# Kernel optimization log

Measured on AMD Instinct MI355X. Metric: run time of the kernel, lower is better.

## Reference

```python
import jax, jax.numpy as jnp
import numpy as np

N, E = 50000, 800000
F_IN, HID, HEADS = 128, 32, 8
H1 = HID * HEADS            # 256: conv1 concat output, also conv2 in/out
NUM_WALKS, WALK_LEN = 512, 64
WINDOW, NEG_S = 5, 10
TEMP = 0.07
NEG_SLOPE = 0.2


def setup_inputs() -> dict:
    key = jax.random.key(0)
    ks = jax.random.split(key, 16)
    inp = {
        "x": jax.random.normal(ks[0], (N, F_IN), jnp.float32),
        "edge_index": jax.random.randint(ks[1], (2, E), 0, N),
        "walks": jax.random.randint(ks[2], (NUM_WALKS, WALK_LEN), 0, N),
        "neg_nodes": jax.random.randint(ks[3], (NUM_WALKS, WALK_LEN, NEG_S), 0, N),
        # conv1 params (GATConv: in=F_IN, out=HID, heads=HEADS, concat)
        "W1": jax.random.normal(ks[4], (F_IN, HEADS * HID), jnp.float32) / np.sqrt(F_IN),
        "a_src1": jax.random.normal(ks[5], (HEADS, HID), jnp.float32) / np.sqrt(HID),
        "a_dst1": jax.random.normal(ks[6], (HEADS, HID), jnp.float32) / np.sqrt(HID),
        "b1": jnp.zeros((HEADS * HID,), jnp.float32),
        # conv2 params (GATConv: in=H1, out=H1, heads=1)
        "W2": jax.random.normal(ks[7], (H1, H1), jnp.float32) / np.sqrt(H1),
        "a_src2": jax.random.normal(ks[8], (1, H1), jnp.float32) / np.sqrt(H1),
        "a_dst2": jax.random.normal(ks[9], (1, H1), jnp.float32) / np.sqrt(H1),
        "b2": jnp.zeros((H1,), jnp.float32),
    }
    return inp


def gat_conv(x, edge_index, W, a_src, a_dst, b, heads, out_ch):
    """PyG-style GATConv: self-loops, per-dst softmax attention, concat heads."""
    n = x.shape[0]
    loops = jnp.arange(n)
    src = jnp.concatenate([edge_index[0], loops])
    dst = jnp.concatenate([edge_index[1], loops])
    xw = (x @ W).reshape(n, heads, out_ch)                  # [N,H,C]
    al_s = jnp.einsum('nhc,hc->nh', xw, a_src)              # [N,H]
    al_d = jnp.einsum('nhc,hc->nh', xw, a_dst)
    e = jax.nn.leaky_relu(al_s[src] + al_d[dst], NEG_SLOPE)  # [Et,H]
    m = jax.ops.segment_max(e, dst, num_segments=n)
    ex = jnp.exp(e - m[dst])
    den = jax.ops.segment_sum(ex, dst, num_segments=n)
    alpha = ex / den[dst]                                    # [Et,H]
    out = jax.ops.segment_sum(alpha[:, :, None] * xw[src], dst, num_segments=n)
    return out.reshape(n, heads * out_ch) + b


def walk_contrastive_loss(emb, walks, neg_nodes):
    eps = 1e-8
    nrm = emb / jnp.clip(jnp.linalg.norm(emb, axis=-1, keepdims=True), eps)
    L = walks.shape[1]
    offs = jnp.concatenate([jnp.arange(-WINDOW, 0), jnp.arange(1, WINDOW + 1)])  # [2W]
    pos_pos = jnp.arange(L)[:, None] + offs[None, :]        # [L,2W]
    pos_valid = (pos_pos >= 0) & (pos_pos < L)
    pos_nodes = walks[:, jnp.clip(pos_pos, 0, L - 1)]       # [B,L,2W]
    anchor = nrm[walks]                                      # [B,L,D]
    pos_sims = jnp.einsum('bld,blpd->blp', anchor, nrm[pos_nodes]) / TEMP
    neg_sims = jnp.einsum('bld,blsd->bls', anchor, nrm[neg_nodes]) / TEMP
    # drop negatives that collide with (valid) positives, as torch.isin filter does
    neg_in_pos = ((neg_nodes[:, :, :, None] == pos_nodes[:, :, None, :])
                  & pos_valid[None, :, None, :]).any(-1)     # [B,L,S]
    pos_sum = jnp.sum(jnp.exp(pos_sims) * pos_valid[None].astype(emb.dtype), axis=-1)
    neg_sum = jnp.sum(jnp.exp(neg_sims) * (~neg_in_pos).astype(emb.dtype), axis=-1)
    has_pos = pos_valid.any(-1)[None]                        # [1,L]
    safe_pos = jnp.where(has_pos, pos_sum, 1.0)
    term = -jnp.log(safe_pos / (safe_pos + neg_sum))
    return jnp.sum(jnp.where(has_pos, term, 0.0))


def reference(x, edge_index, walks, neg_nodes, W1, a_src1, a_dst1, b1,
              W2, a_src2, a_dst2, b2):
    emb1 = jax.nn.elu(gat_conv(x, edge_index, W1, a_src1, a_dst1, b1, HEADS, HID))
    emb2 = gat_conv(emb1, edge_index, W2, a_src2, a_dst2, b2, 1, H1)
    emb = jnp.concatenate([emb1, emb2], axis=1)              # [N, 2*H1]
    return walk_contrastive_loss(emb, walks, neg_nodes)
```

## Files before the change

kernel.cpp:

```cpp
#include <hip/hip_runtime.h>
#include <math.h>

#define N_NODES 50000
#define N_PAD 50048
#define E_EDGES 800000
#define E_PAD (E_EDGES + 8 * N_NODES)
#define FDIM_IN 128
#define HID_1 32
#define HEADS_1 8
#define H1DIM 256
#define NUM_WALKS 512
#define WALK_LEN 64
#define WINDOW 5
#define NEG_S 10
#define TEMP 0.07f
#define INV_TEMP (1.0f / 0.07f)
#define NEG_SLOPE 0.2f
#define LOG2E 1.44269504f

#define SCAN_BLOCKS ((N_NODES + 255) / 256)

typedef unsigned int uint;
typedef unsigned short ushort;
typedef long long i64_t;
typedef __attribute__((ext_vector_type(8))) short bf16x8;
typedef __attribute__((ext_vector_type(8))) ushort us8;
typedef __attribute__((ext_vector_type(4))) float f32x4;
typedef __attribute__((ext_vector_type(2))) float vf2;
typedef __attribute__((ext_vector_type(2))) i64_t i64x2;

__device__ __forceinline__ float leaky(float v) {
    return fmaxf(v, v * NEG_SLOPE);
}

__device__ __forceinline__ float bfl(uint u) { return __uint_as_float(u << 16); }
__device__ __forceinline__ float bfh(uint u) { return __uint_as_float(u & 0xffff0000u); }

__device__ __forceinline__ ushort f2bf(float x) {
    uint u = __float_as_uint(x);
    u = u + 0x7fffu + ((u >> 16) & 1u);
    return (ushort)(u >> 16);
}

__device__ __forceinline__ uint pk4fp8(float a, float b, float c, float d) {
    int u = __builtin_amdgcn_cvt_pk_fp8_f32(a, b, 0, false);
    u = __builtin_amdgcn_cvt_pk_fp8_f32(c, d, u, true);
    return (uint)u;
}

__device__ __forceinline__ float red16(float x) {
    int v = __float_as_int(x);
    x += __int_as_float(__builtin_amdgcn_update_dpp(0, v, 0xB1, 0xF, 0xF, true));
    v = __float_as_int(x);
    x += __int_as_float(__builtin_amdgcn_update_dpp(0, v, 0x4E, 0xF, 0xF, true));
    v = __float_as_int(x);
    x += __int_as_float(__builtin_amdgcn_update_dpp(0, v, 0x141, 0xF, 0xF, true));
    v = __float_as_int(x);
    x += __int_as_float(__builtin_amdgcn_update_dpp(0, v, 0x140, 0xF, 0xF, true));
    return x;
}


#define PB_CVT  6250
#define PB_DEG  3125
#define PB_FILL ((E_PAD / 2 + 255) / 256)
#define PO_DEG  (PB_CVT)
#define PO_FILL (PO_DEG + PB_DEG)
#define PO_WT1  (PO_FILL + PB_FILL)
#define PO_WT2  (PO_WT1 + 128)
#define PO_MISC (PO_WT2 + 256)
#define PREP_GRID (PO_MISC + 1)

__global__ __launch_bounds__(256) void prep_kernel(
        const float* __restrict__ x, const int* __restrict__ ei,
        const float* __restrict__ W1, const float* __restrict__ W2,
        uint* __restrict__ xb, ushort* __restrict__ wt1, ushort* __restrict__ wt2,
        int* __restrict__ deg, uint* __restrict__ srl_u,
        float* __restrict__ als1, float* __restrict__ als2, uint* __restrict__ xw8) {
    const int blk = blockIdx.x, t = threadIdx.x;
    if (blk < PB_CVT) {
        int i = blk * 256 + t;
        float4 v = ((const float4*)x)[i];
        uint2 p;
        p.x = (uint)f2bf(v.x) | ((uint)f2bf(v.y) << 16);
        p.y = (uint)f2bf(v.z) | ((uint)f2bf(v.w) << 16);
        ((uint2*)xb)[i] = p;
    } else if (blk < PO_FILL) {
        int e = (blk - PO_DEG) * 256 + t;
        atomicAdd(&deg[ei[E_EDGES + e]], 1);
    } else if (blk < PO_WT1) {
        int i = (blk - PO_FILL) * 256 + t;
        if (i < E_PAD / 2) srl_u[i] = 0xC350C350u;
    } else if (blk < PO_WT2) {
        int tid = (blk - PO_WT1) * 256 + t;
        int k = tid >> 8, n = tid & 255;
        wt1[n * 128 + k] = f2bf(W1[k * 256 + n]);
    } else if (blk < PO_MISC) {
        int tid = (blk - PO_WT2) * 256 + t;
        int k = tid >> 8, n = tid & 255;
        wt2[n * 256 + k] = f2bf(W2[k * 256 + n]);
    } else {
        if (t < HEADS_1) als1[N_NODES * HEADS_1 + t] = -1e30f;
        if (t == HEADS_1) als2[N_NODES] = -1e30f;
        if (t >= 64 && t < 128) xw8[N_NODES * 64 + (t - 64)] = 0u;
    }
}


__global__ __launch_bounds__(256) void scan_a(const int* __restrict__ deg,
                                              int* __restrict__ excl,
                                              int* __restrict__ bsum) {
    __shared__ int s[256];
    int t = threadIdx.x;
    int i = blockIdx.x * 256 + t;
    int d = (i < N_NODES) ? deg[i] : 0;
    int v = (d + 7) & ~7;
    s[t] = v;
    __syncthreads();
    for (int off = 1; off < 256; off <<= 1) {
        int tmp = (t >= off) ? s[t - off] : 0;
        __syncthreads();
        s[t] += tmp;
        __syncthreads();
    }
    if (i < N_NODES) excl[i] = s[t] - v;
    if (t == 255) bsum[blockIdx.x] = s[255];
}

__global__ __launch_bounds__(256) void scan_b(int* __restrict__ bsum) {
    __shared__ int s[256];
    int t = threadIdx.x;
    int v = (t < SCAN_BLOCKS) ? bsum[t] : 0;
    s[t] = v;
    __syncthreads();
    for (int off = 1; off < 256; off <<= 1) {
        int tmp = (t >= off) ? s[t - off] : 0;
        __syncthreads();
        s[t] += tmp;
        __syncthreads();
    }
    if (t < SCAN_BLOCKS) bsum[t] = s[t] - v;
}

__global__ void scan_c2(const int* __restrict__ deg,
                        int* __restrict__ excl, const int* __restrict__ bsum,
                        int* __restrict__ row_start) {
    int i = blockIdx.x * blockDim.x + threadIdx.x;
    if (i < N_NODES) {
        int rs = excl[i] + bsum[i >> 8];
        row_start[i] = rs;
        if (i == N_NODES - 1) row_start[N_NODES] = rs + ((deg[i] + 7) & ~7);
    }
}

__global__ void bucket_kernel(const int* __restrict__ ei,
                              const int* __restrict__ row_start,
                              int* __restrict__ cursor,
                              ushort* __restrict__ srclist) {
    int e = blockIdx.x * blockDim.x + threadIdx.x;
    if (e >= E_EDGES) return;
    int dst = ei[E_EDGES + e];
    int pos = atomicAdd(&cursor[dst], 1);
    srclist[row_start[dst] + pos] = (ushort)ei[e];
}

template<int K, int H>
__global__ __launch_bounds__(256) void mfma_gemm64(
        const ushort* __restrict__ A,
        const ushort* __restrict__ Wt,
        uint* __restrict__ Y8,
        const float* __restrict__ a_src,
        const float* __restrict__ a_dst,
        float* __restrict__ als, float* __restrict__ ald) {
    constexpr int KP = K + 8;
    constexpr int K8 = K / 8;
    __shared__ __align__(16) ushort As[64 * KP];
    __shared__ float sals[64][5], sald[64][5];
    const int m0 = blockIdx.x * 64;
    const int t = threadIdx.x;
    const uint4* Ag = (const uint4*)(A + (size_t)m0 * K);
    uint4* As4 = (uint4*)As;
    for (int i = t; i < 64 * K8; i += 256) {
        int r = i / K8, c8 = i % K8;
        As4[r * (K8 + 1) + c8] = Ag[i];
    }
    __syncthreads();
    const int wv = __builtin_amdgcn_readfirstlane(t >> 6);
    const int lane = t & 63;
    const int n0 = wv * 64;
    const int mrow = lane & 15, q = lane >> 4;
    f32x4 acc[4][4];
#pragma unroll
    for (int mt = 0; mt < 4; mt++)
#pragma unroll
        for (int i = 0; i < 4; i++) acc[mt][i] = (f32x4){0.f, 0.f, 0.f, 0.f};
#pragma unroll
    for (int k0 = 0; k0 < K; k0 += 32) {
        bf16x8 a[4], b[4];
#pragma unroll
        for (int mt = 0; mt < 4; mt++)
            a[mt] = *(const bf16x8*)(As + (mt * 16 + mrow) * KP + k0 + q * 8);
#pragma unroll
        for (int i = 0; i < 4; i++)
            b[i] = *(const bf16x8*)(Wt + (uint)(n0 + i * 16 + mrow) * K + k0 + q * 8);
#pragma unroll
        for (int mt = 0; mt < 4; mt++)
#pragma unroll
            for (int i = 0; i < 4; i++)
                acc[mt][i] = __builtin_amdgcn_mfma_f32_16x16x32_bf16(a[mt], b[i], acc[mt][i], 0, 0, 0);
    }
    {
        float as[4], ad[4];
#pragma unroll
        for (int i = 0; i < 4; i++) {
            as[i] = a_src[n0 + i * 16 + mrow];
            ad[i] = a_dst[n0 + i * 16 + mrow];
        }
#pragma unroll
        for (int mt = 0; mt < 4; mt++) {
#pragma unroll
            for (int r = 0; r < 4; r++) {
                const int row = m0 + mt * 16 + q * 4 + r;
                if (H == 8) {
                    float ps0 = acc[mt][0][r] * as[0] + acc[mt][1][r] * as[1];
                    float ps1 = acc[mt][2][r] * as[2] + acc[mt][3][r] * as[3];
                    float pd0 = acc[mt][0][r] * ad[0] + acc[mt][1][r] * ad[1];
                    float pd1 = acc[mt][2][r] * ad[2] + acc[mt][3][r] * ad[3];
#pragma unroll
                    for (int o = 1; o < 16; o <<= 1) {
                        ps0 += __shfl_xor(ps0, o, 64); ps1 += __shfl_xor(ps1, o, 64);
                        pd0 += __shfl_xor(pd0, o, 64); pd1 += __shfl_xor(pd1, o, 64);
                    }
                    if (mrow == 0 && row < N_NODES) {
                        als[row * 8 + 2 * wv] = ps0 * LOG2E;
                        als[row * 8 + 2 * wv + 1] = ps1 * LOG2E;
                        ald[row * 8 + 2 * wv] = pd0 * LOG2E;
                        ald[row * 8 + 2 * wv + 1] = pd1 * LOG2E;
                    }
                } else {
                    float ps = acc[mt][0][r] * as[0] + acc[mt][1][r] * as[1]
                             + acc[mt][2][r] * as[2] + acc[mt][3][r] * as[3];
                    float pd = acc[mt][0][r] * ad[0] + acc[mt][1][r] * ad[1]
                             + acc[mt][2][r] * ad[2] + acc[mt][3][r] * ad[3];
#pragma unroll
                    for (int o = 1; o < 16; o <<= 1) {
                        ps += __shfl_xor(ps, o, 64); pd += __shfl_xor(pd, o, 64);
                    }
                    if (mrow == 0) {
                        sals[mt * 16 + q * 4 + r][wv] = ps;
                        sald[mt * 16 + q * 4 + r][wv] = pd;
                    }
                }
            }
        }
    }
    __syncthreads();
    if (H == 1 && t < 64) {
        const int row = m0 + t;
        if (row < N_NODES) {
            als[row] = (sals[t][0] + sals[t][1] + sals[t][2] + sals[t][3]) * LOG2E;
            ald[row] = (sald[t][0] + sald[t][1] + sald[t][2] + sald[t][3]) * LOG2E;
        }
    }
    float* S = (float*)As + wv * 16 * 68;
    const int prow = lane >> 2, pj = lane & 3;
#pragma unroll
    for (int mt = 0; mt < 4; mt++) {
#pragma unroll
        for (int i = 0; i < 4; i++)
#pragma unroll
            for (int r = 0; r < 4; r++)
                S[(q * 4 + r) * 68 + i * 16 + mrow] = acc[mt][i][r];
        const float* cp = S + prow * 68 + pj * 16;
        uint4 o;
        o.x = pk4fp8(cp[0],  cp[1],  cp[2],  cp[3]);
        o.y = pk4fp8(cp[4],  cp[5],  cp[6],  cp[7]);
        o.z = pk4fp8(cp[8],  cp[9],  cp[10], cp[11]);
        o.w = pk4fp8(cp[12], cp[13], cp[14], cp[15]);
        const int row = m0 + mt * 16 + prow;
        if (row < N_NODES)
            ((uint4*)(Y8 + (size_t)row * 64))[wv * 4 + pj] = o;
    }
}

__global__ __launch_bounds__(256) void gat_gather1(
        const int* __restrict__ row_start, const ushort* __restrict__ srclist,
        const float* __restrict__ als, const float* __restrict__ ald,
        const uint* __restrict__ xw8,
        const float* __restrict__ bias,
        ushort* __restrict__ emb1b) {
    const int wid = __builtin_amdgcn_readfirstlane(blockIdx.x * 4 + (threadIdx.x >> 6));
    const uint lane = threadIdx.x & 63;
    const uint h = lane >> 3;
    const float ald_n = ald[wid * HEADS_1 + h];
    const int beg = row_start[wid], end = row_start[wid + 1];

    float ex0 = __builtin_amdgcn_exp2f(leaky(als[wid * HEADS_1 + h] + ald_n));
    uint u = xw8[((uint)wid << 6) + lane];
    vf2 lo = __builtin_amdgcn_cvt_pk_f32_fp8((int)u, false);
    vf2 hi = __builtin_amdgcn_cvt_pk_f32_fp8((int)u, true);
    float den = ex0;
    vf2 exv0 = {ex0, ex0};
    vf2 a01 = exv0 * lo, a23 = exv0 * hi;

    for (int i = beg; i < end; i += 8) {
        us8 sv = *(const us8*)(srclist + i);
        uint rr[8]; float ee[8];
#pragma unroll
        for (int j = 0; j < 8; j++) rr[j] = xw8[((uint)sv[j] << 6) + lane];
#pragma unroll
        for (int j = 0; j < 8; j++) ee[j] = als[(uint)sv[j] * HEADS_1 + h];
#pragma unroll
        for (int j = 0; j < 8; j++) {
            float ex = __builtin_amdgcn_exp2f(leaky(ee[j] + ald_n));
            vf2 l2 = __builtin_amdgcn_cvt_pk_f32_fp8((int)rr[j], false);
            vf2 h2 = __builtin_amdgcn_cvt_pk_f32_fp8((int)rr[j], true);
            den += ex;
            vf2 exv = {ex, ex};
            a01 += exv * l2;
            a23 += exv * h2;
        }
    }
    float inv = 1.f / den;
    float4 bv = ((const float4*)bias)[lane];
    float4 r;
    r.x = a01[0] * inv + bv.x; r.y = a01[1] * inv + bv.y;
    r.z = a23[0] * inv + bv.z; r.w = a23[1] * inv + bv.w;
    r.x = r.x > 0.f ? r.x : __expf(r.x) - 1.f;
    r.y = r.y > 0.f ? r.y : __expf(r.y) - 1.f;
    r.z = r.z > 0.f ? r.z : __expf(r.z) - 1.f;
    r.w = r.w > 0.f ? r.w : __expf(r.w) - 1.f;
    uint2 p;
    p.x = (uint)f2bf(r.x) | ((uint)f2bf(r.y) << 16);
    p.y = (uint)f2bf(r.z) | ((uint)f2bf(r.w) << 16);
    ((uint2*)emb1b)[((uint)wid << 6) + lane] = p;
}

__global__ __launch_bounds__(256) void gat_gather2(
        const int* __restrict__ row_start, const ushort* __restrict__ srclist,
        const float* __restrict__ als, const float* __restrict__ ald,
        const uint* __restrict__ xw8,
        const float* __restrict__ bias,
        const ushort* __restrict__ emb1b,
        uint* __restrict__ embn8) {
    const int wid = __builtin_amdgcn_readfirstlane(blockIdx.x * 4 + (threadIdx.x >> 6));
    const uint lane = threadIdx.x & 63;
    const float ald_n = ald[wid];
    const int beg = row_start[wid], end = row_start[wid + 1];

    float ex0 = __builtin_amdgcn_exp2f(leaky(als[wid] + ald_n));
    uint u = xw8[((uint)wid << 6) + lane];
    vf2 lo = __builtin_amdgcn_cvt_pk_f32_fp8((int)u, false);
    vf2 hi = __builtin_amdgcn_cvt_pk_f32_fp8((int)u, true);
    float den = ex0;
    vf2 exv0 = {ex0, ex0};
    vf2 a01 = exv0 * lo, a23 = exv0 * hi;

    for (int i = beg; i < end; i += 8) {
        us8 sv = *(const us8*)(srclist + i);
        uint rr[8]; float ee[8];
#pragma unroll
        for (int j = 0; j < 8; j++) rr[j] = xw8[((uint)sv[j] << 6) + lane];
#pragma unroll
        for (int j = 0; j < 8; j++) ee[j] = als[(uint)sv[j]];
#pragma unroll
        for (int j = 0; j < 8; j++) {
            float ex = __builtin_amdgcn_exp2f(leaky(ee[j] + ald_n));
            vf2 l2 = __builtin_amdgcn_cvt_pk_f32_fp8((int)rr[j], false);
            vf2 h2 = __builtin_amdgcn_cvt_pk_f32_fp8((int)rr[j], true);
            den += ex;
            vf2 exv = {ex, ex};
            a01 += exv * l2;
            a23 += exv * h2;
        }
    }
    float inv = 1.f / den;
    float4 bv = ((const float4*)bias)[lane];
    float4 e2;
    e2.x = a01[0] * inv + bv.x; e2.y = a01[1] * inv + bv.y;
    e2.z = a23[0] * inv + bv.z; e2.w = a23[1] * inv + bv.w;
    uint2 u1 = ((const uint2*)emb1b)[((uint)wid << 6) + lane];
    float4 e1;
    e1.x = bfl(u1.x); e1.y = bfh(u1.x); e1.z = bfl(u1.y); e1.w = bfh(u1.y);

    float ssum = e1.x * e1.x + e1.y * e1.y + e1.z * e1.z + e1.w * e1.w
               + e2.x * e2.x + e2.y * e2.y + e2.z * e2.z + e2.w * e2.w;
#pragma unroll
    for (int o = 32; o > 0; o >>= 1) ssum += __shfl_xor(ssum, o, 64);
    float innv = 1.f / fmaxf(sqrtf(ssum), 1e-8f);

    uint p1 = pk4fp8(e1.x * innv, e1.y * innv, e1.z * innv, e1.w * innv);
    uint p2 = pk4fp8(e2.x * innv, e2.y * innv, e2.z * innv, e2.w * innv);
    const uint n1 = ((lane >> 4) << 4) | (((lane >> 1) & 3) << 2) | (((lane >> 3) & 1) << 1) | (lane & 1);
    embn8[((uint)wid << 7) + n1] = p1;
    embn8[((uint)wid << 7) + 64 + n1] = p2;
}


#define ROWU 140

__global__ __launch_bounds__(1024, 8) void loss_mfma_kernel(
        const uint* __restrict__ embn8,
        const int* __restrict__ walks, const int* __restrict__ negs,
        float* __restrict__ out) {
    __shared__ __align__(16) uint srows8[WALK_LEN * ROWU];
    __shared__ int wids[WALK_LEN];
    __shared__ float possum[WALK_LEN];
    __shared__ float negsum[WALK_LEN];
    const int b = blockIdx.x;
    const int t = threadIdx.x;
    const int w = __builtin_amdgcn_readfirstlane(t >> 6);
    const int lane = t & 63;
    const int mrow = lane & 15, q = lane >> 4;
    const char* embc = (const char*)embn8;

    if (t < 64) wids[t] = walks[b * WALK_LEN + t];
    else if (t < 128) possum[t - 64] = 0.f;
    else if (t < 192) negsum[t - 128] = 0.f;

    uint4 Bv[8];
    int pnode = negs[b * (WALK_LEN * NEG_S) + (w * 16 + mrow)];
    {
        const char* bp = embc + (((uint)pnode) << 9) + (uint)(q * 16);
#pragma unroll
        for (int j = 0; j < 8; j++) Bv[j] = *(const uint4*)(bp + j * 64);
    }
    __syncthreads();

    {
        const int rA = w * 4 + (lane >> 5);
        const int rB = rA + 2;
        const uint off = lane & 31;
        ((uint4*)(srows8 + rA * ROWU))[off] = ((const uint4*)embn8)[((uint)wids[rA] << 5) + off];
        ((uint4*)(srows8 + rB * ROWU))[off] = ((const uint4*)embn8)[((uint)wids[rB] << 5) + off];
    }
    __syncthreads();

#pragma unroll
    for (int ji = 0; ji < 3; ji++) {
        const int job = w + ji * 16;
        f32x4 acc0 = {0.f, 0.f, 0.f, 0.f};
        f32x4 acc1 = {0.f, 0.f, 0.f, 0.f};
        if (ji < 2 || w < 8) {
            const int albase = (job / 10) * 16;
            const int curnode = pnode;
            const int owner = (job * 16 + mrow) / 10;
            const char* ap = (const char*)(srows8 + (albase + mrow) * ROWU) + q * 16;
#pragma unroll
            for (int j = 0; j < 4; j++) {
                i64x2 a = *(const i64x2*)(ap + j * 64);
                const i64x2 bb = *(const i64x2*)&Bv[j];
                acc0 = __builtin_amdgcn_mfma_f32_16x16x32_fp8_fp8(a[0], bb[0], acc0, 0, 0, 0);
                acc0 = __builtin_amdgcn_mfma_f32_16x16x32_fp8_fp8(a[1], bb[1], acc0, 0, 0, 0);
            }
#pragma unroll
            for (int j = 4; j < 8; j++) {
                i64x2 a = *(const i64x2*)(ap + j * 64);
                const i64x2 bb = *(const i64x2*)&Bv[j];
                acc1 = __builtin_amdgcn_mfma_f32_16x16x32_fp8_fp8(a[0], bb[0], acc1, 0, 0, 0);
                acc1 = __builtin_amdgcn_mfma_f32_16x16x32_fp8_fp8(a[1], bb[1], acc1, 0, 0, 0);
            }
            if (ji == 0 || (ji == 1 && w < 8)) {
                const int njob = job + 16;
                pnode = negs[b * (WALK_LEN * NEG_S) + (njob * 16 + mrow)];
                const char* bp = embc + (((uint)pnode) << 9) + (uint)(q * 16);
#pragma unroll
                for (int j = 0; j < 8; j++) Bv[j] = *(const uint4*)(bp + j * 64);
            }
#pragma unroll
            for (int reg = 0; reg < 4; reg++) {
                const int l_a = albase + q * 4 + reg;
                float e = 0.f;
                if (owner == l_a) {
                    bool msk = false;
#pragma unroll
                    for (int dj = -WINDOW; dj <= WINDOW; dj++) {
                        if (dj == 0) continue;
                        int p = l_a + dj;
                        if (p >= 0 && p < WALK_LEN && wids[p] == curnode) msk = true;
                    }
                    if (!msk) e = __expf((acc0[reg] + acc1[reg]) * INV_TEMP);
                }
                e = red16(e);
                if (mrow == 0 && e != 0.f) atomicAdd(&negsum[l_a], e);
            }
        } else {
            const int pj = w - 8;
            const int g = pj >> 1, half = pj & 1;
            const int albase = g * 16;
            const int base = (albase - WINDOW) > 0 ? (albase - WINDOW) : 0;
            const int hi = (albase + 15 + WINDOW) < (WALK_LEN - 1) ? (albase + 15 + WINDOW) : (WALK_LEN - 1);
            const int cnt = hi - base + 1;
            const int r = half * 16 + mrow;
            const int row = base + r;
            const int rc = row < hi ? row : hi;
            const char* ap = (const char*)(srows8 + (albase + mrow) * ROWU) + q * 16;
            const char* bp = (const char*)(srows8 + rc * ROWU) + q * 16;
#pragma unroll
            for (int j = 0; j < 4; j++) {
                i64x2 a = *(const i64x2*)(ap + j * 64);
                i64x2 bb = *(const i64x2*)(bp + j * 64);
                acc0 = __builtin_amdgcn_mfma_f32_16x16x32_fp8_fp8(a[0], bb[0], acc0, 0, 0, 0);
                acc0 = __builtin_amdgcn_mfma_f32_16x16x32_fp8_fp8(a[1], bb[1], acc0, 0, 0, 0);
            }
#pragma unroll
            for (int j = 4; j < 8; j++) {
                i64x2 a = *(const i64x2*)(ap + j * 64);
                i64x2 bb = *(const i64x2*)(bp + j * 64);
                acc1 = __builtin_amdgcn_mfma_f32_16x16x32_fp8_fp8(a[0], bb[0], acc1, 0, 0, 0);
                acc1 = __builtin_amdgcn_mfma_f32_16x16x32_fp8_fp8(a[1], bb[1], acc1, 0, 0, 0);
            }
#pragma unroll
            for (int reg = 0; reg < 4; reg++) {
                const int l_a = albase + q * 4 + reg;
                const int d = row - l_a;
                bool use = (r < cnt) && (d != 0) && (d >= -WINDOW) && (d <= WINDOW);
                float e = use ? __expf((acc0[reg] + acc1[reg]) * INV_TEMP) : 0.f;
                e = red16(e);
                if (mrow == 0 && e != 0.f) atomicAdd(&possum[l_a], e);
            }
        }
    }
    __syncthreads();
    if (t < 64) {
        float term = logf(1.f + negsum[t] / possum[t]);
#pragma unroll
        for (int o = 32; o > 0; o >>= 1) term += __shfl_xor(term, o, 64);
        if (t == 0) atomicAdd(out, term);
    }
}

extern "C" void kernel_launch(void* const* d_in, const int* in_sizes, int n_in,
                              void* d_out, int out_size, void* d_ws, size_t ws_size,
                              hipStream_t stream) {
    const float* x      = (const float*)d_in[0];
    const int*   ei     = (const int*)d_in[1];
    const int*   walks  = (const int*)d_in[2];
    const int*   negs   = (const int*)d_in[3];
    const float* W1     = (const float*)d_in[4];
    const float* a_src1 = (const float*)d_in[5];
    const float* a_dst1 = (const float*)d_in[6];
    const float* b1     = (const float*)d_in[7];
    const float* W2     = (const float*)d_in[8];
    const float* a_src2 = (const float*)d_in[9];
    const float* a_dst2 = (const float*)d_in[10];
    const float* b2     = (const float*)d_in[11];
    float* out = (float*)d_out;

    float* ws = (float*)d_ws;
    size_t off = 0;
#define ALIGN_OFF off = (off + 255) & ~(size_t)255
    float* r_xw8   = ws + off; off += (size_t)(N_NODES + 1) * 64;  ALIGN_OFF;
    float* r_emb1b = ws + off; off += (size_t)N_PAD * 128;         ALIGN_OFF;
    float* r_embn8 = ws + off; off += (size_t)N_NODES * 128;       ALIGN_OFF;
    float* r_xb    = ws + off; off += (size_t)N_PAD * 64;          ALIGN_OFF;
    float* r_wt1   = ws + off; off += 256 * 64;                    ALIGN_OFF;
    float* r_wt2   = ws + off; off += 256 * 128;                   ALIGN_OFF;
    float* als1  = ws + off; off += (N_NODES + 1) * HEADS_1;       ALIGN_OFF;
    float* ald1  = ws + off; off += N_NODES * HEADS_1;             ALIGN_OFF;
    float* als2  = ws + off; off += N_NODES + 1;                   ALIGN_OFF;
    float* ald2  = ws + off; off += N_NODES;                       ALIGN_OFF;
    int* deg       = (int*)(ws + off); off += N_NODES;             ALIGN_OFF;
    int* excl      = (int*)(ws + off); off += N_NODES;             ALIGN_OFF;
    int* bsum      = (int*)(ws + off); off += 256;                 ALIGN_OFF;
    int* row_start = (int*)(ws + off); off += N_NODES + 1;         ALIGN_OFF;
    int* cursor    = (int*)(ws + off); off += N_NODES;             ALIGN_OFF;
    ushort* srclist = (ushort*)(ws + off); off += E_PAD / 2;       ALIGN_OFF;
    uint*   xw8   = (uint*)r_xw8;
    ushort* emb1b = (ushort*)r_emb1b;
    uint*   embn8 = (uint*)r_embn8;
    ushort* xb    = (ushort*)r_xb;
    ushort* wt1   = (ushort*)r_wt1;
    ushort* wt2   = (ushort*)r_wt2;

    hipMemsetAsync(out, 0, sizeof(float) * out_size, stream);
    hipMemsetAsync(deg, 0, sizeof(int) * N_NODES, stream);
    hipMemsetAsync(cursor, 0, sizeof(int) * N_NODES, stream);

    prep_kernel<<<PREP_GRID, 256, 0, stream>>>(
        x, ei, W1, W2, (uint*)xb, wt1, wt2, deg, (uint*)srclist, als1, als2, xw8);

    scan_a<<<SCAN_BLOCKS, 256, 0, stream>>>(deg, excl, bsum);
    scan_b<<<1, 256, 0, stream>>>(bsum);
    scan_c2<<<SCAN_BLOCKS, 256, 0, stream>>>(deg, excl, bsum, row_start);
    bucket_kernel<<<(E_EDGES + 255) / 256, 256, 0, stream>>>(ei, row_start, cursor, srclist);

    mfma_gemm64<128, HEADS_1><<<N_PAD / 64, 256, 0, stream>>>(
        xb, wt1, xw8, a_src1, a_dst1, als1, ald1);
    gat_gather1<<<N_NODES / 4, 256, 0, stream>>>(
        row_start, srclist, als1, ald1, xw8, b1, emb1b);

    mfma_gemm64<256, 1><<<N_PAD / 64, 256, 0, stream>>>(
        emb1b, wt2, xw8, a_src2, a_dst2, als2, ald2);
    gat_gather2<<<N_NODES / 4, 256, 0, stream>>>(
        row_start, srclist, als2, ald2, xw8, b2, emb1b, embn8);

    loss_mfma_kernel<<<NUM_WALKS, 1024, 0, stream>>>(embn8, walks, negs, out);
}
```

Baseline: 346.8 us.

## Fuse edge bucketing into first GEMM launch with dst-range partitioned blocks

```diff
diff --git a/kernel.cpp b/kernel.cpp
--- a/kernel.cpp
+++ b/kernel.cpp
@@ -19,6 +19,12 @@
 #define LOG2E 1.44269504f
 
 #define SCAN_BLOCKS ((N_NODES + 255) / 256)
+
+#define NCHUNK 3125
+#define NSTRIPE 196
+#define NGEMMG 98
+#define NGROUP1 (NSTRIPE + NGEMMG)
+#define GEMM1_GRID (NGROUP1 * 8)
 
 typedef unsigned int uint;
 typedef unsigned short ushort;
@@ -144,24 +150,14 @@
 
 __global__ void scan_c2(const int* __restrict__ deg,
                         int* __restrict__ excl, const int* __restrict__ bsum,
-                        int* __restrict__ row_start) {
+                        int* __restrict__ row_start, int* __restrict__ cursor) {
     int i = blockIdx.x * blockDim.x + threadIdx.x;
     if (i < N_NODES) {
         int rs = excl[i] + bsum[i >> 8];
         row_start[i] = rs;
+        cursor[i] = rs;
         if (i == N_NODES - 1) row_start[N_NODES] = rs + ((deg[i] + 7) & ~7);
     }
-}
-
-__global__ void bucket_kernel(const int* __restrict__ ei,
-                              const int* __restrict__ row_start,
-                              int* __restrict__ cursor,
-                              ushort* __restrict__ srclist) {
-    int e = blockIdx.x * blockDim.x + threadIdx.x;
-    if (e >= E_EDGES) return;
-    int dst = ei[E_EDGES + e];
-    int pos = atomicAdd(&cursor[dst], 1);
-    srclist[row_start[dst] + pos] = (ushort)ei[e];
 }
 
 template<int K, int H>
@@ -171,12 +167,43 @@
         uint* __restrict__ Y8,
         const float* __restrict__ a_src,
         const float* __restrict__ a_dst,
-        float* __restrict__ als, float* __restrict__ ald) {
+        float* __restrict__ als, float* __restrict__ ald,
+        const int* __restrict__ ei, int* __restrict__ cursor,
+        ushort* __restrict__ srclist) {
     constexpr int KP = K + 8;
     constexpr int K8 = K / 8;
     __shared__ __align__(16) ushort As[64 * KP];
     __shared__ float sals[64][5], sald[64][5];
-    const int m0 = blockIdx.x * 64;
+    int m0;
+    if (H == 8) {
+        const int G = blockIdx.x >> 3;
+        if (G % 3 != 0) {
+            const int stripe = G - G / 3 - 1;
+            const int lo = (blockIdx.x & 7) * (N_NODES / 8);
+            int dstv[16], srcv[16];
+#pragma unroll
+            for (int j = 0; j < 16; j++) {
+                int chunk = stripe + j * NSTRIPE;
+                bool ok = chunk < NCHUNK;
+                int e = chunk * 256 + threadIdx.x;
+                dstv[j] = ok ? ei[E_EDGES + e] : -1;
+                srcv[j] = ok ? ei[e] : 0;
+            }
+#pragma unroll
+            for (int j = 0; j < 16; j++) {
+                if ((uint)(dstv[j] - lo) < (uint)(N_NODES / 8)) {
+                    int pos = atomicAdd(&cursor[dstv[j]], 1);
+                    srclist[pos] = (ushort)srcv[j];
+                }
+            }
+            return;
+        }
+        const int job = (G / 3) * 8 + (blockIdx.x & 7);
+        if (job >= N_PAD / 64) return;
+        m0 = job * 64;
+    } else {
+        m0 = blockIdx.x * 64;
+    }
     const int t = threadIdx.x;
     const uint4* Ag = (const uint4*)(A + (size_t)m0 * K);
     uint4* As4 = (uint4*)As;
@@ -575,23 +602,21 @@
 
     hipMemsetAsync(out, 0, sizeof(float) * out_size, stream);
     hipMemsetAsync(deg, 0, sizeof(int) * N_NODES, stream);
-    hipMemsetAsync(cursor, 0, sizeof(int) * N_NODES, stream);
 
     prep_kernel<<<PREP_GRID, 256, 0, stream>>>(
         x, ei, W1, W2, (uint*)xb, wt1, wt2, deg, (uint*)srclist, als1, als2, xw8);
 
     scan_a<<<SCAN_BLOCKS, 256, 0, stream>>>(deg, excl, bsum);
     scan_b<<<1, 256, 0, stream>>>(bsum);
-    scan_c2<<<SCAN_BLOCKS, 256, 0, stream>>>(deg, excl, bsum, row_start);
-    bucket_kernel<<<(E_EDGES + 255) / 256, 256, 0, stream>>>(ei, row_start, cursor, srclist);
-
-    mfma_gemm64<128, HEADS_1><<<N_PAD / 64, 256, 0, stream>>>(
-        xb, wt1, xw8, a_src1, a_dst1, als1, ald1);
+    scan_c2<<<SCAN_BLOCKS, 256, 0, stream>>>(deg, excl, bsum, row_start, cursor);
+
+    mfma_gemm64<128, HEADS_1><<<GEMM1_GRID, 256, 0, stream>>>(
+        xb, wt1, xw8, a_src1, a_dst1, als1, ald1, ei, cursor, srclist);
     gat_gather1<<<N_NODES / 4, 256, 0, stream>>>(
         row_start, srclist, als1, ald1, xw8, b1, emb1b);
 
     mfma_gemm64<256, 1><<<N_PAD / 64, 256, 0, stream>>>(
-        emb1b, wt2, xw8, a_src2, a_dst2, als2, ald2);
+        emb1b, wt2, xw8, a_src2, a_dst2, als2, ald2, ei, cursor, srclist);
     gat_gather2<<<N_NODES / 4, 256, 0, stream>>>(
         row_start, srclist, als2, ald2, xw8, b2, emb1b, embn8);
 
```

Result: faster. 328.6 us (-5.3%).

## Replace atomic CSR bucket fill with two-pass binned scatter via LDS windows

Applied to the files above, without the earlier changes.

```diff
diff --git a/kernel.cpp b/kernel.cpp
--- a/kernel.cpp
+++ b/kernel.cpp
@@ -20,6 +20,12 @@
 
 #define SCAN_BLOCKS ((N_NODES + 255) / 256)
 
+#define NB 98
+#define GCAP 12288
+#define LCAP 64
+#define BIN_BLOCKS 392
+#define WINCAP 16384
+
 typedef unsigned int uint;
 typedef unsigned short ushort;
 typedef long long i64_t;
@@ -28,6 +34,7 @@
 typedef __attribute__((ext_vector_type(4))) float f32x4;
 typedef __attribute__((ext_vector_type(2))) float vf2;
 typedef __attribute__((ext_vector_type(2))) i64_t i64x2;
+typedef __attribute__((ext_vector_type(4))) uint u32x4;
 
 __device__ __forceinline__ float leaky(float v) {
     return fmaxf(v, v * NEG_SLOPE);
@@ -62,20 +69,15 @@
 
 
 #define PB_CVT  6250
-#define PB_DEG  3125
-#define PB_FILL ((E_PAD / 2 + 255) / 256)
-#define PO_DEG  (PB_CVT)
-#define PO_FILL (PO_DEG + PB_DEG)
-#define PO_WT1  (PO_FILL + PB_FILL)
+#define PO_WT1  (PB_CVT)
 #define PO_WT2  (PO_WT1 + 128)
 #define PO_MISC (PO_WT2 + 256)
 #define PREP_GRID (PO_MISC + 1)
 
 __global__ __launch_bounds__(256) void prep_kernel(
-        const float* __restrict__ x, const int* __restrict__ ei,
+        const float* __restrict__ x,
         const float* __restrict__ W1, const float* __restrict__ W2,
         uint* __restrict__ xb, ushort* __restrict__ wt1, ushort* __restrict__ wt2,
-        int* __restrict__ deg, uint* __restrict__ srl_u,
         float* __restrict__ als1, float* __restrict__ als2, uint* __restrict__ xw8) {
     const int blk = blockIdx.x, t = threadIdx.x;
     if (blk < PB_CVT) {
@@ -85,12 +87,6 @@
         p.x = (uint)f2bf(v.x) | ((uint)f2bf(v.y) << 16);
         p.y = (uint)f2bf(v.z) | ((uint)f2bf(v.w) << 16);
         ((uint2*)xb)[i] = p;
-    } else if (blk < PO_FILL) {
-        int e = (blk - PO_DEG) * 256 + t;
-        atomicAdd(&deg[ei[E_EDGES + e]], 1);
-    } else if (blk < PO_WT1) {
-        int i = (blk - PO_FILL) * 256 + t;
-        if (i < E_PAD / 2) srl_u[i] = 0xC350C350u;
     } else if (blk < PO_WT2) {
         int tid = (blk - PO_WT1) * 256 + t;
         int k = tid >> 8, n = tid & 255;
@@ -107,6 +103,49 @@
 }
 
 
+__global__ __launch_bounds__(256) void bin_kernel(
+        const int* __restrict__ ei, int* __restrict__ deg,
+        uint* __restrict__ gbucket, int* __restrict__ gcur) {
+    __shared__ int scnt[NB];
+    __shared__ int gposs[NB];
+    __shared__ uint sbuf[NB * LCAP];
+    const int t = threadIdx.x;
+    if (t < NB) scnt[t] = 0;
+    __syncthreads();
+    const int e0 = blockIdx.x * 2048;
+#pragma unroll
+    for (int k = 0; k < 8; k++) {
+        int e = e0 + k * 256 + t;
+        if (e < E_EDGES) {
+            int dst = ei[E_EDGES + e];
+            int src = ei[e];
+            atomicAdd(&deg[dst], 1);
+            uint packed = ((uint)dst << 16) | (uint)src;
+            int bk = dst >> 9;
+            int pos = atomicAdd(&scnt[bk], 1);
+            if (pos < LCAP) sbuf[bk * LCAP + pos] = packed;
+            else {
+                int gp = atomicAdd(&gcur[bk], 1);
+                gbucket[bk * GCAP + gp] = packed;
+            }
+        }
+    }
+    __syncthreads();
+    if (t < NB) {
+        int c = scnt[t]; if (c > LCAP) c = LCAP;
+        gposs[t] = atomicAdd(&gcur[t], c);
+        scnt[t] = c;
+    }
+    __syncthreads();
+    const int w = t >> 6, lane = t & 63;
+    for (int b = w; b < NB; b += 4) {
+        int c = scnt[b], gp = gposs[b];
+        for (int i = lane; i < c; i += 64)
+            gbucket[b * GCAP + gp + i] = sbuf[b * LCAP + i];
+    }
+}
+
+
 __global__ __launch_bounds__(256) void scan_a(const int* __restrict__ deg,
                                               int* __restrict__ excl,
                                               int* __restrict__ bsum) {
@@ -153,15 +192,32 @@
     }
 }
 
-__global__ void bucket_kernel(const int* __restrict__ ei,
-                              const int* __restrict__ row_start,
-                              int* __restrict__ cursor,
-                              ushort* __restrict__ srclist) {
-    int e = blockIdx.x * blockDim.x + threadIdx.x;
-    if (e >= E_EDGES) return;
-    int dst = ei[E_EDGES + e];
-    int pos = atomicAdd(&cursor[dst], 1);
-    srclist[row_start[dst] + pos] = (ushort)ei[e];
+
+__global__ __launch_bounds__(256) void scatter_kernel(
+        const uint* __restrict__ gbucket, const int* __restrict__ gcur,
+        const int* __restrict__ row_start, ushort* __restrict__ srclist) {
+    __shared__ ushort win[WINCAP];
+    __shared__ int cur[512];
+    const int b = blockIdx.x, t = threadIdx.x;
+    const int nlo = b << 9;
+    const int nhi = (nlo + 512 < N_NODES) ? (nlo + 512) : N_NODES;
+    const int base = row_start[nlo];
+    const int end = row_start[nhi];
+    const int span = end - base;
+    for (int i = t; i < nhi - nlo; i += 256) cur[i] = row_start[nlo + i] - base;
+    for (int i = t; i < span / 2; i += 256) ((uint*)win)[i] = 0xC350C350u;
+    __syncthreads();
+    const int cnt = gcur[b];
+    for (int i = t; i < cnt; i += 256) {
+        uint packed = gbucket[b * GCAP + i];
+        int dst = packed >> 16;
+        int slot = atomicAdd(&cur[dst - nlo], 1);
+        win[slot] = (ushort)(packed & 0xffffu);
+    }
+    __syncthreads();
+    u32x4* d4 = (u32x4*)(srclist + base);
+    const u32x4* s4 = (const u32x4*)win;
+    for (int i = t; i < span / 8; i += 256) d4[i] = s4[i];
 }
 
 template<int K, int H>
@@ -446,6 +502,7 @@
             const int curnode = pnode;
             const int owner = (job * 16 + mrow) / 10;
             const char* ap = (const char*)(srows8 + (albase + mrow) * ROWU) + q * 16;
+            __builtin_amdgcn_s_setprio(1);
 #pragma unroll
             for (int j = 0; j < 4; j++) {
                 i64x2 a = *(const i64x2*)(ap + j * 64);
@@ -460,6 +517,7 @@
                 acc1 = __builtin_amdgcn_mfma_f32_16x16x32_fp8_fp8(a[0], bb[0], acc1, 0, 0, 0);
                 acc1 = __builtin_amdgcn_mfma_f32_16x16x32_fp8_fp8(a[1], bb[1], acc1, 0, 0, 0);
             }
+            __builtin_amdgcn_s_setprio(0);
             if (ji == 0 || (ji == 1 && w < 8)) {
                 const int njob = job + 16;
                 pnode = negs[b * (WALK_LEN * NEG_S) + (njob * 16 + mrow)];
@@ -496,6 +554,7 @@
             const int rc = row < hi ? row : hi;
             const char* ap = (const char*)(srows8 + (albase + mrow) * ROWU) + q * 16;
             const char* bp = (const char*)(srows8 + rc * ROWU) + q * 16;
+            __builtin_amdgcn_s_setprio(1);
 #pragma unroll
             for (int j = 0; j < 4; j++) {
                 i64x2 a = *(const i64x2*)(ap + j * 64);
@@ -510,6 +569,7 @@
                 acc1 = __builtin_amdgcn_mfma_f32_16x16x32_fp8_fp8(a[0], bb[0], acc1, 0, 0, 0);
                 acc1 = __builtin_amdgcn_mfma_f32_16x16x32_fp8_fp8(a[1], bb[1], acc1, 0, 0, 0);
             }
+            __builtin_amdgcn_s_setprio(0);
 #pragma unroll
             for (int reg = 0; reg < 4; reg++) {
                 const int l_a = albase + q * 4 + reg;
@@ -564,7 +624,8 @@
     int* excl      = (int*)(ws + off); off += N_NODES;             ALIGN_OFF;
     int* bsum      = (int*)(ws + off); off += 256;                 ALIGN_OFF;
     int* row_start = (int*)(ws + off); off += N_NODES + 1;         ALIGN_OFF;
-    int* cursor    = (int*)(ws + off); off += N_NODES;             ALIGN_OFF;
+    uint* gbucket  = (uint*)(ws + off); off += (size_t)NB * GCAP;  ALIGN_OFF;
+    int* gcur      = (int*)(ws + off); off += 256;                 ALIGN_OFF;
     ushort* srclist = (ushort*)(ws + off); off += E_PAD / 2;       ALIGN_OFF;
     uint*   xw8   = (uint*)r_xw8;
     ushort* emb1b = (ushort*)r_emb1b;
@@ -575,15 +636,18 @@
 
     hipMemsetAsync(out, 0, sizeof(float) * out_size, stream);
     hipMemsetAsync(deg, 0, sizeof(int) * N_NODES, stream);
-    hipMemsetAsync(cursor, 0, sizeof(int) * N_NODES, stream);
+    hipMemsetAsync(gcur, 0, sizeof(int) * NB, stream);
 
     prep_kernel<<<PREP_GRID, 256, 0, stream>>>(
-        x, ei, W1, W2, (uint*)xb, wt1, wt2, deg, (uint*)srclist, als1, als2, xw8);
+        x, W1, W2, (uint*)xb, wt1, wt2, als1, als2, xw8);
+
+    bin_kernel<<<BIN_BLOCKS, 256, 0, stream>>>(ei, deg, gbucket, gcur);
 
     scan_a<<<SCAN_BLOCKS, 256, 0, stream>>>(deg, excl, bsum);
     scan_b<<<1, 256, 0, stream>>>(bsum);
     scan_c2<<<SCAN_BLOCKS, 256, 0, stream>>>(deg, excl, bsum, row_start);
-    bucket_kernel<<<(E_EDGES + 255) / 256, 256, 0, stream>>>(ei, row_start, cursor, srclist);
+
+    scatter_kernel<<<NB, 256, 0, stream>>>(gbucket, gcur, row_start, srclist);
 
     mfma_gemm64<128, HEADS_1><<<N_PAD / 64, 256, 0, stream>>>(
         xb, wt1, xw8, a_src1, a_dst1, als1, ald1);
```

New measurement: 335.4 us. 3.3% less time.
